# Performance work log

Hardware: AMD Instinct MI355X
Metric: run time of the kernel (lower is better)

The kernel has to match this reference:

```python
import jax, jax.numpy as jnp
import numpy as np

B, V, D, H, A = 512, 64, 32, 64, 8  # batch, num_vars, input_dim, hidden, out_dim
E = V * (V - 1)
HALF_LOG_2PI = 0.5 * float(np.log(2.0 * np.pi))
LOG2 = float(np.log(2.0))


def setup_inputs() -> dict:
    key = jax.random.key(0)
    ks = jax.random.split(key, 16)
    adj = np.ones((V, V)) - np.eye(V)
    send, recv = np.where(adj)
    s = 0.05
    return {
        "inputs": jax.random.normal(ks[0], (B, V, D), jnp.float32),
        "edges": jax.random.uniform(ks[1], (B, E, 2), jnp.float32),
        "m1_w": jax.random.normal(ks[2], (2 * D, H), jnp.float32) * s,
        "m1_b": jax.random.normal(ks[3], (H,), jnp.float32) * s,
        "m2_w": jax.random.normal(ks[4], (H, H), jnp.float32) * s,
        "m2_b": jax.random.normal(ks[5], (H,), jnp.float32) * s,
        "fc1_w": jax.random.normal(ks[6], (D + H, H), jnp.float32) * s,
        "fc1_b": jax.random.normal(ks[7], (H,), jnp.float32) * s,
        "fc2_w": jax.random.normal(ks[8], (H, H), jnp.float32) * s,
        "fc2_b": jax.random.normal(ks[9], (H,), jnp.float32) * s,
        "mu_w": jax.random.normal(ks[10], (H, A), jnp.float32) * 0.003,
        "mu_b": jax.random.normal(ks[11], (A,), jnp.float32) * 0.003,
        "ls_w": jax.random.normal(ks[12], (H, A), jnp.float32) * s,
        "ls_b": jax.random.normal(ks[13], (A,), jnp.float32) * s,
        "send_e": jnp.asarray(send, jnp.int32),
        "recv_e": jnp.asarray(recv, jnp.int32),
    }


def reference(inputs, edges, m1_w, m1_b, m2_w, m2_b, fc1_w, fc1_b,
              fc2_w, fc2_b, mu_w, mu_b, ls_w, ls_b, send_e, recv_e):
    # --- GNN message passing (eval mode: dropout p=0; skip edge type 0) ---
    pre_msg = jnp.concatenate(
        [inputs[:, recv_e, :], inputs[:, send_e, :]], axis=-1)  # [B,E,2D]
    h = jax.nn.relu(pre_msg @ m1_w + m1_b)                      # [B,E,H]
    msg = jax.nn.relu(h @ m2_w + m2_b) * edges[:, :, 1:2]       # [B,E,H]
    # edge2node onehot matmul == scatter-sum over receiver index
    agg = jnp.zeros((inputs.shape[0], inputs.shape[1], msg.shape[-1]),
                    msg.dtype).at[:, recv_e, :].add(msg)        # [B,V,H]
    aug = jnp.concatenate([inputs, agg], axis=-1)               # [B,V,D+H]
    # --- Policy head (eval: pi_action = mu) ---
    h1 = jax.nn.relu(aug @ fc1_w + fc1_b)
    h2 = jax.nn.relu(h1 @ fc2_w + fc2_b)
    mu = h2 @ mu_w + mu_b                                       # [B,V,A]
    log_std = jnp.clip(h2 @ ls_w + ls_b, -3.0, 1.0)
    # Normal(mu, std).log_prob(mu) = -log(std) - 0.5*log(2*pi)
    logp = jnp.sum(-log_std - HALF_LOG_2PI, axis=-1)            # [B,V]
    logp = logp - jnp.sum(
        2.0 * (LOG2 - mu - jax.nn.softplus(-2.0 * mu)), axis=-1)
    return jnp.tanh(mu), logp, aug
```

## Files before the change

### kernel.cpp

```cpp
#include <hip/hip_runtime.h>

#define NB 512
#define NV 64
#define ND 32
#define NH 64
#define NE 4032

typedef short s16x8 __attribute__((ext_vector_type(8)));
typedef float f32x4 __attribute__((ext_vector_type(4)));
typedef unsigned int u32;

#define HLOG2PI 0.9189385332046727f
#define LOG2C   0.6931471805599453f

__device__ __forceinline__ unsigned short f2bf(float f){
  u32 u = __float_as_uint(f);
  u += 0x7FFFu + ((u >> 16) & 1u);
  return (unsigned short)(u >> 16);
}
__device__ __forceinline__ u32 pk2(float a, float b){
  return (u32)f2bf(a) | ((u32)f2bf(b) << 16);
}
__device__ __forceinline__ void gload16(const void* g, void* l){
  __builtin_amdgcn_global_load_lds(
      (const __attribute__((address_space(1))) void*)g,
      (__attribute__((address_space(3))) void*)l, 16, 0, 0);
}


__global__ __launch_bounds__(256) void k_setup(
    const int* __restrict__ recv, const int* __restrict__ send,
    const float* __restrict__ x,
    const float* __restrict__ m1w, const float* __restrict__ m2w,
    const float* __restrict__ f1w, const float* __restrict__ f2w,
    const float* __restrict__ muw, const float* __restrict__ lsw,
    int* __restrict__ ebyv, int* __restrict__ sbyv,
    unsigned short* __restrict__ Wg, unsigned short* __restrict__ Fg,
    uint4* __restrict__ xbf)
{
  const int blk = blockIdx.x, t = threadIdx.x;
  if (blk == 0){
    __shared__ int cnt[NV];
    if (t < NV) cnt[t] = 0;
    __syncthreads();
    for (int e = t; e < NE; e += 256){
      int v = recv[e];
      int p = atomicAdd(&cnt[v], 1);
      ebyv[v*64 + p] = e;
      sbyv[v*64 + p] = send[e];
    }
    __syncthreads();
    if (t < NV){
      for (int s = cnt[t]; s < 64; s++){ ebyv[t*64 + s] = -1; sbyv[t*64 + s] = t; }
    }
  } else if (blk == 1){
    #pragma unroll
    for (int i = 0; i < 8; i++){ int idx = i*256 + t; int kk = idx>>6, j = idx&63;
      Wg[j*32 + (((kk>>3) ^ ((j>>1)&3))<<3) + (kk&7)] = f2bf(m1w[(32+kk)*64 + j]); }
  } else if (blk == 2){
    #pragma unroll
    for (int i = 0; i < 16; i++){ int idx = i*256 + t; int k = idx>>6, j = idx&63;
      Wg[2048 + j*64 + (((k>>3)^(j&7))<<3) + (k&7)] = f2bf(m2w[idx]); }
  } else if (blk == 3){
    #pragma unroll
    for (int i = 0; i < 24; i++){ int idx = i*256 + t; int k = idx>>6, j = idx&63;
      Fg[j*128 + (((k>>3)^(j&7))<<3) + (k&7)] = f2bf(f1w[idx]); }
  } else if (blk == 4){
    #pragma unroll
    for (int i = 0; i < 16; i++){ int idx = i*256 + t; int k = idx>>6, j = idx&63;
      Fg[8192 + j*64 + (((k>>3)^(j&7))<<3) + (k&7)] = f2bf(f2w[idx]); }
  } else if (blk == 5){
    #pragma unroll
    for (int i = 0; i < 4; i++){ int idx = i*256 + t; int k = idx>>4, j = idx&15;
      float s = (j < 8) ? muw[k*8 + j] : lsw[k*8 + (j-8)];
      Fg[12288 + j*64 + (((k>>3)^(j&7))<<3) + (k&7)] = f2bf(s); }
  } else {
    int i = (blk - 6)*256 + t;
    const float4* s = (const float4*)x + i*2;
    float4 a = s[0], b = s[1];
    xbf[i] = make_uint4(pk2(a.x,a.y), pk2(a.z,a.w), pk2(b.x,b.y), pk2(b.z,b.w));
  }
}


__global__ __launch_bounds__(256, 3) void k_msg(
    const unsigned short* __restrict__ xbf, const float* __restrict__ x,
    const float* __restrict__ edges,
    const int* __restrict__ ebyv, const int* __restrict__ sbyv,
    const unsigned short* __restrict__ Wg, const float* __restrict__ m1w,
    const float* __restrict__ b1g, const float* __restrict__ b2g,
    float* __restrict__ out_aug)
{
  __shared__ __align__(16) unsigned short WlA[6144];
  __shared__ __align__(16) char Hx[4][4096];
  __shared__ float wrowS[4][64];
  __shared__ float b1e[4][64];
  __shared__ float agg[4][64];

  const int tid = threadIdx.x;
  const int w = tid >> 6, lane = tid & 63;
  const int l16 = lane & 15, l4 = lane >> 4;
  const int v = blockIdx.x & 63, bg = blockIdx.x >> 6;
  const int b = bg*4 + w;

  #pragma unroll
  for (int i = 0; i < 3; i++)
    gload16(Wg + (i*256 + tid)*8, (char*)WlA + i*4096 + w*1024);

  int sv[4];
  #pragma unroll
  for (int il = 0; il < 4; il++) sv[il] = sbyv[v*64 + il*16 + l16];
  s16x8 xf[4];
  #pragma unroll
  for (int il = 0; il < 4; il++)
    xf[il] = *(const s16x8*)(xbf + (b*NV + sv[il])*32 + l4*8);

  { int e = ebyv[v*64 + lane];
    wrowS[w][lane] = (e >= 0) ? edges[(b*NE + e)*2 + 1] : 0.0f; }

  { float s = b1g[lane];
    const float* xr = x + (b*NV + v)*ND;
    #pragma unroll
    for (int k = 0; k < 32; k++) s = fmaf(xr[k], m1w[k*64 + lane], s);
    b1e[w][lane] = s; }

  __syncthreads();

  const int ch32 = (l4 ^ ((l16 >> 1) & 3)) << 3;
  const int sw8  = l16 & 7;
  char* Hw = Hx[w];
  const unsigned short* Wl2 = WlA + 2048;

  f32x4 acc2[4][4] = {};
  #pragma unroll
  for (int half = 0; half < 2; half++){
    f32x4 a1[2][4] = {};
    #pragma unroll
    for (int jm = 0; jm < 2; jm++){
      s16x8 af = *(const s16x8*)(WlA + ((half*2 + jm)*16 + l16)*32 + ch32);
      #pragma unroll
      for (int il = 0; il < 4; il++)
        a1[jm][il] = __builtin_amdgcn_mfma_f32_16x16x32_bf16(af, xf[il], a1[jm][il], 0, 0, 0);
    }
    #pragma unroll
    for (int jm = 0; jm < 2; jm++){
      float4 bq = *(const float4*)&b1e[w][(half*2 + jm)*16 + l4*4];
      #pragma unroll
      for (int il = 0; il < 4; il++){
        float h0 = fmaxf(a1[jm][il][0] + bq.x, 0.0f);
        float h1 = fmaxf(a1[jm][il][1] + bq.y, 0.0f);
        float h2 = fmaxf(a1[jm][il][2] + bq.z, 0.0f);
        float h3 = fmaxf(a1[jm][il][3] + bq.w, 0.0f);
        *(uint2*)(Hw + il*1024 + (jm*2 + (l4 >> 1))*256 + l16*16 + (l4 & 1)*8) =
            make_uint2(pk2(h0, h1), pk2(h2, h3));
      }
    }
    __builtin_amdgcn_sched_barrier(0);
    s16x8 hf[4], wf[4];
    #pragma unroll
    for (int im = 0; im < 4; im++)
      hf[im] = *(const s16x8*)(Hw + im*1024 + lane*16);
    #pragma unroll
    for (int jt = 0; jt < 4; jt++)
      wf[jt] = *(const s16x8*)(Wl2 + (jt*16 + l16)*64 + (((half*4 + l4) ^ sw8) << 3));
    #pragma unroll
    for (int im = 0; im < 4; im++)
      #pragma unroll
      for (int jt = 0; jt < 4; jt++)
        acc2[im][jt] = __builtin_amdgcn_mfma_f32_16x16x32_bf16(hf[im], wf[jt], acc2[im][jt], 0, 0, 0);
    __builtin_amdgcn_sched_barrier(0);
  }

  {
    float4 wq[4];
    #pragma unroll
    for (int im = 0; im < 4; im++) wq[im] = *(const float4*)&wrowS[w][im*16 + l4*4];
    #pragma unroll
    for (int jt = 0; jt < 4; jt++){
      float b2v = b2g[jt*16 + l16];
      float s = 0.0f;
      #pragma unroll
      for (int im = 0; im < 4; im++){
        s += fmaxf(acc2[im][jt][0] + b2v, 0.0f) * wq[im].x;
        s += fmaxf(acc2[im][jt][1] + b2v, 0.0f) * wq[im].y;
        s += fmaxf(acc2[im][jt][2] + b2v, 0.0f) * wq[im].z;
        s += fmaxf(acc2[im][jt][3] + b2v, 0.0f) * wq[im].w;
      }
      s += __shfl_xor(s, 16);
      s += __shfl_xor(s, 32);
      if (l4 == 0) agg[w][jt*16 + l16] = s;
    }
  }
  __builtin_amdgcn_sched_barrier(0);
  {
    int rowg = b*NV + v;
    out_aug[rowg*96 + 32 + lane] = agg[w][lane];
    if (lane < 32) out_aug[rowg*96 + lane] = x[rowg*ND + lane];
  }
}


__global__ __launch_bounds__(256) void k_node(
    const float* __restrict__ aug,
    const unsigned short* __restrict__ Fg,
    const float* __restrict__ f1b, const float* __restrict__ f2b,
    const float* __restrict__ mub, const float* __restrict__ lsb,
    float* __restrict__ out0, float* __restrict__ out1)
{
  __shared__ __align__(16) unsigned short Wn[1664*8];
  __shared__ __align__(16) char Hn[4][2048];
  const unsigned short* F1 = Wn;
  const unsigned short* F2 = Wn + 8192;
  const unsigned short* HW = Wn + 12288;

  const int tid = threadIdx.x;
  const int w = tid >> 6, lane = tid & 63;
  const int l16 = lane & 15, l4 = lane >> 4;
  const int row = blockIdx.x*64 + w*16 + l16;

  #pragma unroll
  for (int i = 0; i < 7; i++){
    if (i*256 + w*64 < 1664)
      gload16(Fg + (i*256 + w*64 + lane)*8, (char*)Wn + i*4096 + w*1024);
  }
  s16x8 bf1[3];
  #pragma unroll
  for (int ks = 0; ks < 3; ks++){
    const float4* p = (const float4*)(aug + row*96 + (ks*4 + l4)*8);
    float4 a = p[0], c = p[1];
    union { uint4 q; s16x8 v; } uu;
    uu.q = make_uint4(pk2(a.x,a.y), pk2(a.z,a.w), pk2(c.x,c.y), pk2(c.z,c.w));
    bf1[ks] = uu.v;
  }
  __syncthreads();

  const int sw8 = l16 & 7;
  char* Hw = Hn[w];

  f32x4 a1[4] = {};
  #pragma unroll
  for (int ks = 0; ks < 3; ks++)
    #pragma unroll
    for (int jt = 0; jt < 4; jt++){
      s16x8 af = *(const s16x8*)(F1 + (jt*16 + l16)*128 + (((ks*4 + l4) ^ sw8) << 3));
      a1[jt] = __builtin_amdgcn_mfma_f32_16x16x32_bf16(af, bf1[ks], a1[jt], 0, 0, 0);
    }
  #pragma unroll
  for (int jt = 0; jt < 4; jt++){
    float4 bq = *(const float4*)(f1b + jt*16 + l4*4);
    float h0 = fmaxf(a1[jt][0] + bq.x, 0.0f);
    float h1 = fmaxf(a1[jt][1] + bq.y, 0.0f);
    float h2 = fmaxf(a1[jt][2] + bq.z, 0.0f);
    float h3 = fmaxf(a1[jt][3] + bq.w, 0.0f);
    *(uint2*)(Hw + (jt >> 1)*1024 + ((jt & 1)*2 + (l4 >> 1))*256 + l16*16 + (l4 & 1)*8) =
        make_uint2(pk2(h0, h1), pk2(h2, h3));
  }
  __builtin_amdgcn_sched_barrier(0);
  s16x8 bh[2];
  bh[0] = *(const s16x8*)(Hw + lane*16);
  bh[1] = *(const s16x8*)(Hw + 1024 + lane*16);
  f32x4 a2[4] = {};
  #pragma unroll
  for (int ks = 0; ks < 2; ks++)
    #pragma unroll
    for (int jt = 0; jt < 4; jt++){
      s16x8 af = *(const s16x8*)(F2 + (jt*16 + l16)*64 + (((ks*4 + l4) ^ sw8) << 3));
      a2[jt] = __builtin_amdgcn_mfma_f32_16x16x32_bf16(af, bh[ks], a2[jt], 0, 0, 0);
    }
  __builtin_amdgcn_sched_barrier(0);
  #pragma unroll
  for (int jt = 0; jt < 4; jt++){
    float4 bq = *(const float4*)(f2b + jt*16 + l4*4);
    float h0 = fmaxf(a2[jt][0] + bq.x, 0.0f);
    float h1 = fmaxf(a2[jt][1] + bq.y, 0.0f);
    float h2 = fmaxf(a2[jt][2] + bq.z, 0.0f);
    float h3 = fmaxf(a2[jt][3] + bq.w, 0.0f);
    *(uint2*)(Hw + (jt >> 1)*1024 + ((jt & 1)*2 + (l4 >> 1))*256 + l16*16 + (l4 & 1)*8) =
        make_uint2(pk2(h0, h1), pk2(h2, h3));
  }
  __builtin_amdgcn_sched_barrier(0);
  bh[0] = *(const s16x8*)(Hw + lane*16);
  bh[1] = *(const s16x8*)(Hw + 1024 + lane*16);
  f32x4 a3 = {};
  #pragma unroll
  for (int ks = 0; ks < 2; ks++){
    s16x8 af = *(const s16x8*)(HW + l16*64 + (((ks*4 + l4) ^ sw8) << 3));
    a3 = __builtin_amdgcn_mfma_f32_16x16x32_bf16(af, bh[ks], a3, 0, 0, 0);
  }
  float term = 0.0f;
  if (l4 < 2){
    float4 t;
    #pragma unroll
    for (int r = 0; r < 4; r++){
      int o = l4*4 + r;
      float mu = a3[r] + mub[o];
      ((float*)&t)[r] = tanhf(mu);
      float xm = -2.0f * mu;
      float sp = fmaxf(xm, 0.0f) + log1pf(expf(-fabsf(xm)));
      term += -2.0f * (LOG2C - mu - sp);
    }
    *(float4*)(out0 + row*8 + l4*4) = t;
  } else {
    #pragma unroll
    for (int r = 0; r < 4; r++){
      float lsv = fminf(fmaxf(a3[r] + lsb[l4*4 + r - 8], -3.0f), 1.0f);
      term += -lsv - HLOG2PI;
    }
  }
  term += __shfl_xor(term, 16);
  term += __shfl_xor(term, 32);
  if (l4 == 0) out1[row] = term;
}


extern "C" void kernel_launch(void* const* d_in, const int* in_sizes, int n_in,
                              void* d_out, int out_size, void* d_ws, size_t ws_size,
                              hipStream_t stream) {
  const float* x     = (const float*)d_in[0];
  const float* edges = (const float*)d_in[1];
  const float* m1w   = (const float*)d_in[2];
  const float* m1b   = (const float*)d_in[3];
  const float* m2w   = (const float*)d_in[4];
  const float* m2b   = (const float*)d_in[5];
  const float* f1w   = (const float*)d_in[6];
  const float* f1b   = (const float*)d_in[7];
  const float* f2w   = (const float*)d_in[8];
  const float* f2b   = (const float*)d_in[9];
  const float* muw   = (const float*)d_in[10];
  const float* mub   = (const float*)d_in[11];
  const float* lsw   = (const float*)d_in[12];
  const float* lsb   = (const float*)d_in[13];
  const int*   send  = (const int*)d_in[14];
  const int*   recv  = (const int*)d_in[15];

  char* ws = (char*)d_ws;
  int* ebyv = (int*)ws;
  int* sbyv = (int*)(ws + 16384);
  unsigned short* Wg  = (unsigned short*)(ws + 32768);
  unsigned short* Fg  = (unsigned short*)(ws + 49152);
  unsigned short* xbf = (unsigned short*)(ws + 75776);

  float* out0    = (float*)d_out;
  float* out1    = out0 + NB*NV*8;
  float* out_aug = out1 + NB*NV;

  k_setup<<<6 + NB*NV*ND/2048, 256, 0, stream>>>(recv, send, x, m1w, m2w,
                                                 f1w, f2w, muw, lsw,
                                                 ebyv, sbyv, Wg, Fg, (uint4*)xbf);
  k_msg<<<NB*NV/4, 256, 0, stream>>>(xbf, x, edges, ebyv, sbyv, Wg, m1w,
                                     m1b, m2b, out_aug);
  k_node<<<NB*NV/64, 256, 0, stream>>>(out_aug, Fg, f1b, f2b, mub, lsb, out0, out1);
}
```

Baseline: 163.9 us.

## Split edge-weight gather into separate kernel and read weights directly from global

Moves the strided edge-weight gather out of the message kernel into a new k_gather kernel that writes a compact per-node weight buffer. The message kernel drops the LDS staging of the m1/m2 weights and reads MFMA operands straight from global memory with unswizzled layouts. It also splits each node's 64 edges across two waves, cutting registers and raising the occupancy target, and adds priority hints around the MFMA blocks. In exchange it adds an extra kernel launch, a round trip through the workspace, and a block-wide barrier to combine partial sums.

```diff
diff --git a/kernel.cpp b/kernel.cpp
--- a/kernel.cpp
+++ b/kernel.cpp
@@ -56,11 +56,11 @@
   } else if (blk == 1){
     #pragma unroll
     for (int i = 0; i < 8; i++){ int idx = i*256 + t; int kk = idx>>6, j = idx&63;
-      Wg[j*32 + (((kk>>3) ^ ((j>>1)&3))<<3) + (kk&7)] = f2bf(m1w[(32+kk)*64 + j]); }
+      Wg[j*32 + kk] = f2bf(m1w[(32+kk)*64 + j]); }
   } else if (blk == 2){
     #pragma unroll
     for (int i = 0; i < 16; i++){ int idx = i*256 + t; int k = idx>>6, j = idx&63;
-      Wg[2048 + j*64 + (((k>>3)^(j&7))<<3) + (k&7)] = f2bf(m2w[idx]); }
+      Wg[2048 + j*64 + k] = f2bf(m2w[k*64 + j]); }
   } else if (blk == 3){
     #pragma unroll
     for (int i = 0; i < 24; i++){ int idx = i*256 + t; int k = idx>>6, j = idx&63;
@@ -83,70 +83,73 @@
 }
 
 
-__global__ __launch_bounds__(256, 3) void k_msg(
+__global__ __launch_bounds__(256) void k_gather(
+    const float* __restrict__ edges, const int* __restrict__ ebyv,
+    float* __restrict__ wgt)
+{
+  const int v = blockIdx.x & 63, b4 = blockIdx.x >> 6;
+  const int slot = threadIdx.x & 63, w = threadIdx.x >> 6;
+  const int b = b4*4 + w;
+  int e = ebyv[v*64 + slot];
+  float val = (e >= 0) ? edges[(b*NE + e)*2 + 1] : 0.0f;
+  wgt[(b*64 + v)*64 + slot] = val;
+}
+
+
+__global__ __launch_bounds__(256, 4) void k_msg(
     const unsigned short* __restrict__ xbf, const float* __restrict__ x,
-    const float* __restrict__ edges,
-    const int* __restrict__ ebyv, const int* __restrict__ sbyv,
+    const float* __restrict__ wgt,
+    const int* __restrict__ sbyv,
     const unsigned short* __restrict__ Wg, const float* __restrict__ m1w,
     const float* __restrict__ b1g, const float* __restrict__ b2g,
     float* __restrict__ out_aug)
 {
-  __shared__ __align__(16) unsigned short WlA[6144];
-  __shared__ __align__(16) char Hx[4][4096];
-  __shared__ float wrowS[4][64];
-  __shared__ float b1e[4][64];
-  __shared__ float agg[4][64];
+  __shared__ __align__(16) char Hx[4][2048];
+  __shared__ float b1eS[4][64];
+  __shared__ float aggP[4][64];
 
   const int tid = threadIdx.x;
   const int w = tid >> 6, lane = tid & 63;
   const int l16 = lane & 15, l4 = lane >> 4;
-  const int v = blockIdx.x & 63, bg = blockIdx.x >> 6;
-  const int b = bg*4 + w;
-
-  #pragma unroll
-  for (int i = 0; i < 3; i++)
-    gload16(Wg + (i*256 + tid)*8, (char*)WlA + i*4096 + w*1024);
-
-  int sv[4];
-  #pragma unroll
-  for (int il = 0; il < 4; il++) sv[il] = sbyv[v*64 + il*16 + l16];
-  s16x8 xf[4];
-  #pragma unroll
-  for (int il = 0; il < 4; il++)
-    xf[il] = *(const s16x8*)(xbf + (b*NV + sv[il])*32 + l4*8);
-
-  { int e = ebyv[v*64 + lane];
-    wrowS[w][lane] = (e >= 0) ? edges[(b*NE + e)*2 + 1] : 0.0f; }
-
-  { float s = b1g[lane];
-    const float* xr = x + (b*NV + v)*ND;
-    #pragma unroll
+  const int v = blockIdx.x & 63, bg2 = blockIdx.x >> 6;
+  const int b = bg2*2 + (w >> 1);
+  const int rh = w & 1;
+  const int rowg = b*NV + v;
+
+  int sv0 = sbyv[v*64 + rh*32 + l16];
+  int sv1 = sbyv[v*64 + rh*32 + 16 + l16];
+  s16x8 xf0 = *(const s16x8*)(xbf + (b*NV + sv0)*32 + l4*8);
+  s16x8 xf1 = *(const s16x8*)(xbf + (b*NV + sv1)*32 + l4*8);
+
+  {
+    float s = b1g[lane];
+    const float* xr = x + rowg*ND;
+    #pragma unroll 8
     for (int k = 0; k < 32; k++) s = fmaf(xr[k], m1w[k*64 + lane], s);
-    b1e[w][lane] = s; }
-
-  __syncthreads();
-
-  const int ch32 = (l4 ^ ((l16 >> 1) & 3)) << 3;
-  const int sw8  = l16 & 7;
+    b1eS[w][lane] = s;
+  }
+
+  const unsigned short* W1bg = Wg;
+  const unsigned short* W2g  = Wg + 2048;
   char* Hw = Hx[w];
-  const unsigned short* Wl2 = WlA + 2048;
-
-  f32x4 acc2[4][4] = {};
+
+  f32x4 acc2[2][4] = {};
   #pragma unroll
   for (int half = 0; half < 2; half++){
-    f32x4 a1[2][4] = {};
+    f32x4 a1[2][2] = {};
+    __builtin_amdgcn_s_setprio(1);
     #pragma unroll
     for (int jm = 0; jm < 2; jm++){
-      s16x8 af = *(const s16x8*)(WlA + ((half*2 + jm)*16 + l16)*32 + ch32);
+      s16x8 af = *(const s16x8*)(W1bg + (half*32 + jm*16 + l16)*32 + l4*8);
+      a1[jm][0] = __builtin_amdgcn_mfma_f32_16x16x32_bf16(af, xf0, a1[jm][0], 0, 0, 0);
+      a1[jm][1] = __builtin_amdgcn_mfma_f32_16x16x32_bf16(af, xf1, a1[jm][1], 0, 0, 0);
+    }
+    __builtin_amdgcn_s_setprio(0);
+    #pragma unroll
+    for (int jm = 0; jm < 2; jm++){
+      float4 bq = *(const float4*)&b1eS[w][half*32 + jm*16 + l4*4];
       #pragma unroll
-      for (int il = 0; il < 4; il++)
-        a1[jm][il] = __builtin_amdgcn_mfma_f32_16x16x32_bf16(af, xf[il], a1[jm][il], 0, 0, 0);
-    }
-    #pragma unroll
-    for (int jm = 0; jm < 2; jm++){
-      float4 bq = *(const float4*)&b1e[w][(half*2 + jm)*16 + l4*4];
-      #pragma unroll
-      for (int il = 0; il < 4; il++){
+      for (int il = 0; il < 2; il++){
         float h0 = fmaxf(a1[jm][il][0] + bq.x, 0.0f);
         float h1 = fmaxf(a1[jm][il][1] + bq.y, 0.0f);
         float h2 = fmaxf(a1[jm][il][2] + bq.z, 0.0f);
@@ -156,45 +159,42 @@
       }
     }
     __builtin_amdgcn_sched_barrier(0);
-    s16x8 hf[4], wf[4];
-    #pragma unroll
-    for (int im = 0; im < 4; im++)
-      hf[im] = *(const s16x8*)(Hw + im*1024 + lane*16);
-    #pragma unroll
-    for (int jt = 0; jt < 4; jt++)
-      wf[jt] = *(const s16x8*)(Wl2 + (jt*16 + l16)*64 + (((half*4 + l4) ^ sw8) << 3));
-    #pragma unroll
-    for (int im = 0; im < 4; im++)
-      #pragma unroll
-      for (int jt = 0; jt < 4; jt++)
-        acc2[im][jt] = __builtin_amdgcn_mfma_f32_16x16x32_bf16(hf[im], wf[jt], acc2[im][jt], 0, 0, 0);
+    s16x8 hf0 = *(const s16x8*)(Hw + lane*16);
+    s16x8 hf1 = *(const s16x8*)(Hw + 1024 + lane*16);
+    __builtin_amdgcn_s_setprio(1);
+    #pragma unroll
+    for (int jt = 0; jt < 4; jt++){
+      s16x8 wf = *(const s16x8*)(W2g + (jt*16 + l16)*64 + (half*4 + l4)*8);
+      acc2[0][jt] = __builtin_amdgcn_mfma_f32_16x16x32_bf16(hf0, wf, acc2[0][jt], 0, 0, 0);
+      acc2[1][jt] = __builtin_amdgcn_mfma_f32_16x16x32_bf16(hf1, wf, acc2[1][jt], 0, 0, 0);
+    }
+    __builtin_amdgcn_s_setprio(0);
     __builtin_amdgcn_sched_barrier(0);
   }
 
   {
-    float4 wq[4];
-    #pragma unroll
-    for (int im = 0; im < 4; im++) wq[im] = *(const float4*)&wrowS[w][im*16 + l4*4];
+    float4 wq0 = *(const float4*)(wgt + rowg*64 + rh*32 + l4*4);
+    float4 wq1 = *(const float4*)(wgt + rowg*64 + rh*32 + 16 + l4*4);
     #pragma unroll
     for (int jt = 0; jt < 4; jt++){
       float b2v = b2g[jt*16 + l16];
-      float s = 0.0f;
-      #pragma unroll
-      for (int im = 0; im < 4; im++){
-        s += fmaxf(acc2[im][jt][0] + b2v, 0.0f) * wq[im].x;
-        s += fmaxf(acc2[im][jt][1] + b2v, 0.0f) * wq[im].y;
-        s += fmaxf(acc2[im][jt][2] + b2v, 0.0f) * wq[im].z;
-        s += fmaxf(acc2[im][jt][3] + b2v, 0.0f) * wq[im].w;
-      }
+      float s = fmaxf(acc2[0][jt][0] + b2v, 0.0f) * wq0.x
+              + fmaxf(acc2[0][jt][1] + b2v, 0.0f) * wq0.y
+              + fmaxf(acc2[0][jt][2] + b2v, 0.0f) * wq0.z
+              + fmaxf(acc2[0][jt][3] + b2v, 0.0f) * wq0.w
+              + fmaxf(acc2[1][jt][0] + b2v, 0.0f) * wq1.x
+              + fmaxf(acc2[1][jt][1] + b2v, 0.0f) * wq1.y
+              + fmaxf(acc2[1][jt][2] + b2v, 0.0f) * wq1.z
+              + fmaxf(acc2[1][jt][3] + b2v, 0.0f) * wq1.w;
       s += __shfl_xor(s, 16);
       s += __shfl_xor(s, 32);
-      if (l4 == 0) agg[w][jt*16 + l16] = s;
-    }
-  }
-  __builtin_amdgcn_sched_barrier(0);
-  {
-    int rowg = b*NV + v;
-    out_aug[rowg*96 + 32 + lane] = agg[w][lane];
+      if (l4 == 0) aggP[w][jt*16 + l16] = s;
+    }
+  }
+  __syncthreads();
+  if ((w & 1) == 0){
+    float sum = aggP[w][lane] + aggP[w + 1][lane];
+    out_aug[rowg*96 + 32 + lane] = sum;
     if (lane < 32) out_aug[rowg*96 + lane] = x[rowg*ND + lane];
   }
 }
@@ -339,6 +339,7 @@
   unsigned short* Wg  = (unsigned short*)(ws + 32768);
   unsigned short* Fg  = (unsigned short*)(ws + 49152);
   unsigned short* xbf = (unsigned short*)(ws + 75776);
+  float* wgt          = (float*)(ws + 2172928);
 
   float* out0    = (float*)d_out;
   float* out1    = out0 + NB*NV*8;
@@ -347,7 +348,8 @@
   k_setup<<<6 + NB*NV*ND/2048, 256, 0, stream>>>(recv, send, x, m1w, m2w,
                                                  f1w, f2w, muw, lsw,
                                                  ebyv, sbyv, Wg, Fg, (uint4*)xbf);
-  k_msg<<<NB*NV/4, 256, 0, stream>>>(xbf, x, edges, ebyv, sbyv, Wg, m1w,
-                                     m1b, m2b, out_aug);
+  k_gather<<<(NB/4)*NV, 256, 0, stream>>>(edges, ebyv, wgt);
+  k_msg<<<(NB/2)*NV, 256, 0, stream>>>(xbf, x, wgt, sbyv, Wg, m1w,
+                                       m1b, m2b, out_aug);
   k_node<<<NB*NV/64, 256, 0, stream>>>(out_aug, Fg, f1b, f2b, mub, lsb, out0, out1);
 }
```

Result: slower. 253.4 us (+54.6%).
